# Kernel tuning notes

Hardware: AMD Instinct MI355X
Metric: run time of the kernel (lower is better)

## Reference

```python
import jax, jax.numpy as jnp
import numpy as np

B, S, D = 2, 2048, 1024
HEADS, HEAD_DIM = 16, 64

def setup_inputs() -> dict:
    key = jax.random.key(0)
    ks = jax.random.split(key, 5)
    sc = 0.02
    return {
        "hidden_states": jax.random.normal(ks[0], (B, S, D), jnp.float32),
        "Wq": jax.random.normal(ks[1], (D, HEADS * HEAD_DIM), jnp.float32) * sc,
        "Wk": jax.random.normal(ks[2], (D, HEADS * HEAD_DIM), jnp.float32) * sc,
        "Wv": jax.random.normal(ks[3], (D, HEADS * HEAD_DIM), jnp.float32) * sc,
        "Wo": jax.random.normal(ks[4], (HEADS * HEAD_DIM, D), jnp.float32) * sc,
        "bo": jnp.zeros((D,), jnp.float32),
    }

def reference(hidden_states, Wq, Wk, Wv, Wo, bo):
    b, s, _ = hidden_states.shape
    # QKV projections (no bias, as in diffusers Attention defaults)
    q = (hidden_states @ Wq).reshape(b, s, HEADS, HEAD_DIM).transpose(0, 2, 1, 3)
    k = (hidden_states @ Wk).reshape(b, s, HEADS, HEAD_DIM).transpose(0, 2, 1, 3)
    v = (hidden_states @ Wv).reshape(b, s, HEADS, HEAD_DIM).transpose(0, 2, 1, 3)
    scale = 1.0 / jnp.sqrt(jnp.asarray(HEAD_DIM, hidden_states.dtype))
    scores = jnp.einsum('bhqd,bhkd->bhqk', q, k) * scale  # full NxN scores
    attn = jax.nn.softmax(scores, axis=-1)
    out = jnp.einsum('bhqk,bhkd->bhqd', attn, v)
    out = out.transpose(0, 2, 1, 3).reshape(b, s, HEADS * HEAD_DIM)
    return out @ Wo + bo
```

## Files before the change

kernel.cpp:

```cpp
#include <hip/hip_runtime.h>

#define B_ 2
#define S_ 2048
#define D_ 1024
#define H_ 16
#define HD_ 64
#define M_ (B_ * S_)

typedef __attribute__((ext_vector_type(4))) float f32x4;
typedef __attribute__((ext_vector_type(16))) float f32x16;
typedef __attribute__((ext_vector_type(8))) short s16x8;
typedef unsigned short u16;
typedef unsigned int u32;

#define QSCALE 0.1803368801111204f

__device__ __forceinline__ u16 f2bf(float f) {
  unsigned u = __float_as_uint(f);
  u += 0x7fffu + ((u >> 16) & 1u);
  return (u16)(u >> 16);
}

__device__ __forceinline__ u32 cvtpk_bf16(float lo, float hi) {
  u32 r;
  asm("v_cvt_pk_bf16_f32 %0, %1, %2" : "=v"(r) : "v"(lo), "v"(hi));
  return r;
}

__device__ __forceinline__ void g2lds16(const u16* g, u16* l) {
  __builtin_amdgcn_global_load_lds((const __attribute__((address_space(1))) u32*)(g),
                                   (__attribute__((address_space(3))) u32*)(l), 16, 0, 0);
}

__global__ __launch_bounds__(256) void prep_kernel(
    const float* __restrict__ X, const float* __restrict__ Wq,
    const float* __restrict__ Wk, const float* __restrict__ Wv,
    const float* __restrict__ Wo, u16* __restrict__ Xb, u16* __restrict__ Wt0) {
  __shared__ float tile[32][33];
  const int id = blockIdx.x;
  if (id < 2048) {
    int i = (id * 256 + threadIdx.x) * 8;
    const float4 va = *(const float4*)(X + i);
    const float4 vb = *(const float4*)(X + i + 4);
    union { u32 u[4]; s16x8 v; } pk;
    pk.u[0] = cvtpk_bf16(va.x, va.y); pk.u[1] = cvtpk_bf16(va.z, va.w);
    pk.u[2] = cvtpk_bf16(vb.x, vb.y); pk.u[3] = cvtpk_bf16(vb.z, vb.w);
    *(s16x8*)(Xb + i) = pk.v;
    return;
  }
  const int id2 = id - 2048;
  const int z = id2 >> 10;
  const float* W = (z == 0) ? Wq : (z == 1) ? Wk : (z == 2) ? Wv : Wo;
  u16* Wt = Wt0 + (size_t)z * (D_ * D_);
  const float sc = (z == 0) ? QSCALE : 1.0f;
  const int tx = threadIdx.x & 31, ty = threadIdx.x >> 5;
  const int c0 = (id2 & 31) * 32, r0 = ((id2 >> 5) & 31) * 32;
#pragma unroll
  for (int j = 0; j < 32; j += 8)
    tile[ty + j][tx] = W[(size_t)(r0 + ty + j) * D_ + c0 + tx];
  __syncthreads();
#pragma unroll
  for (int j = 0; j < 32; j += 8)
    Wt[(size_t)(c0 + ty + j) * D_ + r0 + tx] = f2bf(tile[tx][ty + j] * sc);
}

__global__ __launch_bounds__(256) void gemm_qkv_kernel(
    const u16* __restrict__ Xb, const u16* __restrict__ WqT,
    const u16* __restrict__ WkT, const u16* __restrict__ WvT,
    u16* __restrict__ Qb, u16* __restrict__ Kb, u16* __restrict__ Vt) {
  __shared__ u16 As[2][128 * 32];
  __shared__ u16 Bs[2][128 * 32];
  const int tid = threadIdx.x;
  const int lane = tid & 63, wid = tid >> 6;
  const int wr = wid >> 1, wc = wid & 1;
  const int l15 = lane & 15, l4 = lane >> 4;
  const int bm = blockIdx.x * 128;
  const int bn128 = blockIdx.y;
  const int sel = bn128 >> 3;
  const u16* Wt = (sel == 0) ? WqT : (sel == 1) ? WkT : WvT;
  const int bn = (bn128 & 7) * 128;
  const int r0 = lane >> 2;
  const int c0 = lane & 3;

#define GSTAGE(buf, kt)                                                          \
  do {                                                                           \
    _Pragma("unroll") for (int j = 0; j < 2; ++j) {                              \
      const int row = (wid * 2 + j) * 16 + r0;                                   \
      g2lds16(Xb + (size_t)(bm + row) * D_ + (kt) + c0 * 8,                      \
              &As[buf][(wid * 2 + j) * 512]);                                    \
      g2lds16(Wt + (size_t)(bn + row) * D_ + (kt) + c0 * 8,                      \
              &Bs[buf][(wid * 2 + j) * 512]);                                    \
    }                                                                            \
  } while (0)

  f32x4 acc[4][4] = {};
  GSTAGE(0, 0);
  __syncthreads();
  int cur = 0;
  for (int kt = 0; kt < D_; kt += 32) {
    GSTAGE(cur ^ 1, (kt + 32) & (D_ - 1));
    s16x8 af[4], bfr[4];
#pragma unroll
    for (int i = 0; i < 4; ++i) af[i] = *(const s16x8*)&As[cur][(wr * 64 + i * 16 + l15) * 32 + l4 * 8];
#pragma unroll
    for (int j = 0; j < 4; ++j) bfr[j] = *(const s16x8*)&Bs[cur][(wc * 64 + j * 16 + l15) * 32 + l4 * 8];
#pragma unroll
    for (int i = 0; i < 4; ++i)
#pragma unroll
      for (int j = 0; j < 4; ++j)
        acc[i][j] = __builtin_amdgcn_mfma_f32_16x16x32_bf16(af[i], bfr[j], acc[i][j], 0, 0, 0);
    __syncthreads();
    cur ^= 1;
  }
#undef GSTAGE
#pragma unroll
  for (int i = 0; i < 4; ++i)
#pragma unroll
    for (int j = 0; j < 4; ++j)
#pragma unroll
      for (int r = 0; r < 4; ++r) {
        int m = bm + wr * 64 + i * 16 + l4 * 4 + r;
        int n = bn + wc * 64 + j * 16 + l15;
        int bb = m >> 11, s = m & (S_ - 1);
        int h = n >> 6, d = n & 63;
        u16 v = f2bf(acc[i][j][r]);
        size_t bhsel = (size_t)bb * H_ + h;
        if (sel == 0)      Qb[(bhsel * S_ + s) * HD_ + d] = v;
        else if (sel == 1) Kb[(bhsel * S_ + s) * HD_ + d] = v;
        else               Vt[(bhsel * HD_ + d) * S_ + s] = v;
      }
}

__global__ __launch_bounds__(512, 2) void attn_kernel(
    const u16* __restrict__ Qb, const u16* __restrict__ Kb,
    const u16* __restrict__ Vt, u16* __restrict__ Ob) {
  __shared__ char smem_raw[65536];
  typedef u16 (*lds_t)[2][4096];
  lds_t Ks = (lds_t)smem_raw;
  lds_t Vs = (lds_t)(smem_raw + 32768);
  const int tid = threadIdx.x;
  const int lane = tid & 63, wid = tid >> 6;
  const int qg = wid & 3, half = wid >> 2;
  const int l31 = lane & 31, hi = lane >> 5;
  const int id = blockIdx.x;
  const int bh = (id & 7) * 4 + (id >> 6);
  const int qx = (id >> 3) & 7;
  const size_t kbase = (size_t)bh * S_ * HD_;
  const size_t vbase = (size_t)bh * HD_ * S_;
  const int q0 = qx * 256 + qg * 64;
  const int r0 = lane >> 3;
  const int cs = ((lane & 7) ^ r0) * 8;
  const int kv0 = half << 10;

#define STAGE(buf, kvv)                                                          \
  do {                                                                           \
    _Pragma("unroll") for (int j = 0; j < 2; ++j) {                              \
      const int row = (qg * 2 + j) * 8 + r0;                                     \
      g2lds16(Kb + kbase + (size_t)((kvv) + row) * HD_ + cs,                     \
              &Ks[half][buf][(qg * 2 + j) * 512]);                               \
      g2lds16(Vt + vbase + (size_t)row * S_ + (kvv) + cs,                        \
              &Vs[half][buf][(qg * 2 + j) * 512]);                               \
    }                                                                            \
  } while (0)

  STAGE(0, kv0);

  s16x8 aqA[4], aqB[4];
#pragma unroll
  for (int kc = 0; kc < 4; ++kc) {
    aqA[kc] = *(const s16x8*)(Qb + kbase + (size_t)(q0 + l31) * HD_ + kc * 16 + hi * 8);
    aqB[kc] = *(const s16x8*)(Qb + kbase + (size_t)(q0 + 32 + l31) * HD_ + kc * 16 + hi * 8);
  }

  f32x16 accA0 = {}, accA1 = {}, accB0 = {}, accB1 = {};
  float lsA = 0.f, lsB = 0.f;

  int choff[4];
#pragma unroll
  for (int c = 0; c < 4; ++c) choff[c] = ((c * 2 + hi) ^ (l31 & 7)) * 8;

  __syncthreads();

  for (int t = 0; t < 16; ++t) {
    const int buf = t & 1;
    STAGE(buf ^ 1, kv0 + (((t + 1) & 15) << 6));

    f32x16 sA0 = {}, sA1 = {}, sB0 = {}, sB1 = {};
    __builtin_amdgcn_s_setprio(1);
#pragma unroll
    for (int kc = 0; kc < 4; ++kc) {
      const s16x8 ka0 = *(const s16x8*)&Ks[half][buf][(l31) * 64 + choff[kc]];
      const s16x8 ka1 = *(const s16x8*)&Ks[half][buf][(32 + l31) * 64 + choff[kc]];
      sA0 = __builtin_amdgcn_mfma_f32_32x32x16_bf16(ka0, aqA[kc], sA0, 0, 0, 0);
      sB0 = __builtin_amdgcn_mfma_f32_32x32x16_bf16(ka0, aqB[kc], sB0, 0, 0, 0);
      sA1 = __builtin_amdgcn_mfma_f32_32x32x16_bf16(ka1, aqA[kc], sA1, 0, 0, 0);
      sB1 = __builtin_amdgcn_mfma_f32_32x32x16_bf16(ka1, aqB[kc], sB1, 0, 0, 0);
    }
    __builtin_amdgcn_s_setprio(0);

    float tA = 0.f, tB = 0.f;
#pragma unroll
    for (int r = 0; r < 16; ++r) {
      sA0[r] = __builtin_amdgcn_exp2f(sA0[r]);
      sA1[r] = __builtin_amdgcn_exp2f(sA1[r]);
      sB0[r] = __builtin_amdgcn_exp2f(sB0[r]);
      sB1[r] = __builtin_amdgcn_exp2f(sB1[r]);
      tA += sA0[r] + sA1[r];
      tB += sB0[r] + sB1[r];
    }
    lsA += tA;
    lsB += tB;

    s16x8 paA[4], paB[4];
#pragma unroll
    for (int c = 0; c < 4; ++c) {
      const int rr = (c & 1) * 8;
      u32 a0, a1, b0, b1;
      if (c < 2) {
        a0 = cvtpk_bf16(sA0[rr + 0], sA0[rr + 1]);
        a1 = cvtpk_bf16(sA0[rr + 2], sA0[rr + 3]);
        b0 = cvtpk_bf16(sA0[rr + 4], sA0[rr + 5]);
        b1 = cvtpk_bf16(sA0[rr + 6], sA0[rr + 7]);
      } else {
        a0 = cvtpk_bf16(sA1[rr + 0], sA1[rr + 1]);
        a1 = cvtpk_bf16(sA1[rr + 2], sA1[rr + 3]);
        b0 = cvtpk_bf16(sA1[rr + 4], sA1[rr + 5]);
        b1 = cvtpk_bf16(sA1[rr + 6], sA1[rr + 7]);
      }
      asm volatile("v_permlane32_swap_b32 %0, %1" : "+v"(a0), "+v"(b0));
      asm volatile("v_permlane32_swap_b32 %0, %1" : "+v"(a1), "+v"(b1));
      union { u32 u[4]; s16x8 v; } pk;
      pk.u[0] = a0; pk.u[1] = a1; pk.u[2] = b0; pk.u[3] = b1;
      paA[c] = pk.v;
    }
#pragma unroll
    for (int c = 0; c < 4; ++c) {
      const int rr = (c & 1) * 8;
      u32 a0, a1, b0, b1;
      if (c < 2) {
        a0 = cvtpk_bf16(sB0[rr + 0], sB0[rr + 1]);
        a1 = cvtpk_bf16(sB0[rr + 2], sB0[rr + 3]);
        b0 = cvtpk_bf16(sB0[rr + 4], sB0[rr + 5]);
        b1 = cvtpk_bf16(sB0[rr + 6], sB0[rr + 7]);
      } else {
        a0 = cvtpk_bf16(sB1[rr + 0], sB1[rr + 1]);
        a1 = cvtpk_bf16(sB1[rr + 2], sB1[rr + 3]);
        b0 = cvtpk_bf16(sB1[rr + 4], sB1[rr + 5]);
        b1 = cvtpk_bf16(sB1[rr + 6], sB1[rr + 7]);
      }
      asm volatile("v_permlane32_swap_b32 %0, %1" : "+v"(a0), "+v"(b0));
      asm volatile("v_permlane32_swap_b32 %0, %1" : "+v"(a1), "+v"(b1));
      union { u32 u[4]; s16x8 v; } pk;
      pk.u[0] = a0; pk.u[1] = a1; pk.u[2] = b0; pk.u[3] = b1;
      paB[c] = pk.v;
    }

    __builtin_amdgcn_s_setprio(1);
#pragma unroll
    for (int c = 0; c < 4; ++c) {
      const s16x8 vb0 = *(const s16x8*)&Vs[half][buf][(l31) * 64 + choff[c]];
      const s16x8 vb1 = *(const s16x8*)&Vs[half][buf][(32 + l31) * 64 + choff[c]];
      accA0 = __builtin_amdgcn_mfma_f32_32x32x16_bf16(paA[c], vb0, accA0, 0, 0, 0);
      accB0 = __builtin_amdgcn_mfma_f32_32x32x16_bf16(paB[c], vb0, accB0, 0, 0, 0);
      accA1 = __builtin_amdgcn_mfma_f32_32x32x16_bf16(paA[c], vb1, accA1, 0, 0, 0);
      accB1 = __builtin_amdgcn_mfma_f32_32x32x16_bf16(paB[c], vb1, accB1, 0, 0, 0);
    }
    __builtin_amdgcn_s_setprio(0);

    __syncthreads();
  }
#undef STAGE

  lsA += __shfl_xor(lsA, 32);
  lsB += __shfl_xor(lsB, 32);
  const int bb = bh >> 4, h = bh & 15;
  float (*MB)[64][33] = (float(*)[64][33])smem_raw;

  if (half) {
#pragma unroll
    for (int r = 0; r < 16; ++r) {
      MB[qg][lane][r] = accA0[r];
      MB[qg][lane][16 + r] = accA1[r];
    }
    MB[qg][lane][32] = lsA;
  }
  __syncthreads();
  if (!half) {
    lsA += MB[qg][lane][32];
#pragma unroll
    for (int r = 0; r < 16; ++r) {
      accA0[r] += MB[qg][lane][r];
      accA1[r] += MB[qg][lane][16 + r];
    }
#pragma unroll
    for (int r = 0; r < 16; ++r) {
      const int qrow = (r & 3) + 8 * (r >> 2) + 4 * hi;
      const float rinv = 1.0f / __shfl(lsA, qrow);
      const int q = q0 + qrow;
      Ob[(size_t)(bb * S_ + q) * (H_ * HD_) + h * HD_ + l31] = f2bf(accA0[r] * rinv);
      Ob[(size_t)(bb * S_ + q) * (H_ * HD_) + h * HD_ + 32 + l31] = f2bf(accA1[r] * rinv);
    }
  }
  __syncthreads();
  if (half) {
#pragma unroll
    for (int r = 0; r < 16; ++r) {
      MB[qg][lane][r] = accB0[r];
      MB[qg][lane][16 + r] = accB1[r];
    }
    MB[qg][lane][32] = lsB;
  }
  __syncthreads();
  if (!half) {
    lsB += MB[qg][lane][32];
#pragma unroll
    for (int r = 0; r < 16; ++r) {
      accB0[r] += MB[qg][lane][r];
      accB1[r] += MB[qg][lane][16 + r];
    }
#pragma unroll
    for (int r = 0; r < 16; ++r) {
      const int qrow = (r & 3) + 8 * (r >> 2) + 4 * hi;
      const float rinv = 1.0f / __shfl(lsB, qrow);
      const int q = q0 + 32 + qrow;
      Ob[(size_t)(bb * S_ + q) * (H_ * HD_) + h * HD_ + l31] = f2bf(accB0[r] * rinv);
      Ob[(size_t)(bb * S_ + q) * (H_ * HD_) + h * HD_ + 32 + l31] = f2bf(accB1[r] * rinv);
    }
  }
}

__global__ __launch_bounds__(256, 2) void gemm_o_kernel(
    const u16* __restrict__ A, const u16* __restrict__ Bt,
    const float* __restrict__ bias, float* __restrict__ C) {
  __shared__ u16 As[2][128 * 32];
  __shared__ u16 Bs[2][64 * 32];
  const int tid = threadIdx.x;
  const int lane = tid & 63, wid = tid >> 6;
  const int l15 = lane & 15, l4 = lane >> 4;
  const int bm = blockIdx.x * 128;
  const int bn = blockIdx.y * 64;
  const int r0 = lane >> 2;
  const int c0 = lane & 3;

#define GSTAGE(buf, kt)                                                          \
  do {                                                                           \
    _Pragma("unroll") for (int j = 0; j < 2; ++j) {                              \
      const int row = (wid * 2 + j) * 16 + r0;                                   \
      g2lds16(A + (size_t)(bm + row) * D_ + (kt) + c0 * 8,                       \
              &As[buf][(wid * 2 + j) * 512]);                                    \
    }                                                                            \
    g2lds16(Bt + (size_t)(bn + wid * 16 + r0) * D_ + (kt) + c0 * 8,              \
            &Bs[buf][wid * 512]);                                                \
  } while (0)

  f32x4 acc[2][4] = {};
  GSTAGE(0, 0);
  __syncthreads();
  int cur = 0;
  for (int kt = 0; kt < D_; kt += 32) {
    GSTAGE(cur ^ 1, (kt + 32) & (D_ - 1));
    s16x8 af[2], bfr[4];
#pragma unroll
    for (int i = 0; i < 2; ++i) af[i] = *(const s16x8*)&As[cur][(wid * 32 + i * 16 + l15) * 32 + l4 * 8];
#pragma unroll
    for (int j = 0; j < 4; ++j) bfr[j] = *(const s16x8*)&Bs[cur][(j * 16 + l15) * 32 + l4 * 8];
#pragma unroll
    for (int i = 0; i < 2; ++i)
#pragma unroll
      for (int j = 0; j < 4; ++j)
        acc[i][j] = __builtin_amdgcn_mfma_f32_16x16x32_bf16(af[i], bfr[j], acc[i][j], 0, 0, 0);
    __syncthreads();
    cur ^= 1;
  }
#undef GSTAGE
#pragma unroll
  for (int i = 0; i < 2; ++i)
#pragma unroll
    for (int j = 0; j < 4; ++j)
#pragma unroll
      for (int r = 0; r < 4; ++r) {
        int m = bm + wid * 32 + i * 16 + l4 * 4 + r;
        int n = bn + j * 16 + l15;
        C[(size_t)m * D_ + n] = acc[i][j][r] + bias[n];
      }
}

extern "C" void kernel_launch(void* const* d_in, const int* in_sizes, int n_in,
                              void* d_out, int out_size, void* d_ws, size_t ws_size,
                              hipStream_t stream) {
  const float* X  = (const float*)d_in[0];
  const float* Wq = (const float*)d_in[1];
  const float* Wk = (const float*)d_in[2];
  const float* Wv = (const float*)d_in[3];
  const float* Wo = (const float*)d_in[4];
  const float* bo = (const float*)d_in[5];
  float* out = (float*)d_out;

  char* w = (char*)d_ws;
  u16* Xb  = (u16*)(w);
  u16* WT  = (u16*)(w + (8u << 20));
  u16* WqT = WT;
  u16* WkT = WT + (1u << 20);
  u16* WvT = WT + (2u << 20);
  u16* WoT = WT + (3u << 20);
  u16* Qb  = (u16*)(w + (16u << 20));
  u16* Kb  = (u16*)(w + (24u << 20));
  u16* Vt  = (u16*)(w + (32u << 20));
  u16* Ob  = (u16*)(w + (40u << 20));

  prep_kernel<<<6144, 256, 0, stream>>>(X, Wq, Wk, Wv, Wo, Xb, WT);
  gemm_qkv_kernel<<<dim3(32, 24), 256, 0, stream>>>(Xb, WqT, WkT, WvT, Qb, Kb, Vt);
  attn_kernel<<<256, 512, 0, stream>>>(Qb, Kb, Vt, Ob);
  gemm_o_kernel<<<dim3(32, 16), 256, 0, stream>>>(Ob, WoT, bo, out);
}
```

Measured before the change: 113.6 us.

## Compute softmax row sums via MFMA with ones and stage V transpose through LDS

The attention kernel drops the per-element VALU summation of exponentiated scores. Row sums are now accumulated by extra MFMA calls that multiply the bf16 probabilities by a vector of ones, and the final reduction reads the sums straight from the accumulator layout, so no shuffle is needed. The QKV GEMM epilogue for V now writes the transposed tile through swizzled shared memory and stores 16-byte coalesced rows instead of scattered 2-byte writes. The costs are two extra MFMAs per PV step, a larger LDS reduction buffer, and row sums taken from bf16-rounded probabilities rather than fp32 values.

```diff
diff --git a/kernel.cpp b/kernel.cpp
--- a/kernel.cpp
+++ b/kernel.cpp
@@ -68,8 +68,9 @@
     const u16* __restrict__ Xb, const u16* __restrict__ WqT,
     const u16* __restrict__ WkT, const u16* __restrict__ WvT,
     u16* __restrict__ Qb, u16* __restrict__ Kb, u16* __restrict__ Vt) {
-  __shared__ u16 As[2][128 * 32];
-  __shared__ u16 Bs[2][128 * 32];
+  __shared__ u16 ldsraw[16384];
+  u16 (*As)[4096] = (u16(*)[4096])ldsraw;
+  u16 (*Bs)[4096] = (u16(*)[4096])(ldsraw + 8192);
   const int tid = threadIdx.x;
   const int lane = tid & 63, wid = tid >> 6;
   const int wr = wid >> 1, wc = wid & 1;
@@ -113,22 +114,49 @@
     cur ^= 1;
   }
 #undef GSTAGE
-#pragma unroll
-  for (int i = 0; i < 4; ++i)
-#pragma unroll
-    for (int j = 0; j < 4; ++j)
-#pragma unroll
-      for (int r = 0; r < 4; ++r) {
-        int m = bm + wr * 64 + i * 16 + l4 * 4 + r;
-        int n = bn + wc * 64 + j * 16 + l15;
-        int bb = m >> 11, s = m & (S_ - 1);
-        int h = n >> 6, d = n & 63;
-        u16 v = f2bf(acc[i][j][r]);
-        size_t bhsel = (size_t)bb * H_ + h;
-        if (sel == 0)      Qb[(bhsel * S_ + s) * HD_ + d] = v;
-        else if (sel == 1) Kb[(bhsel * S_ + s) * HD_ + d] = v;
-        else               Vt[(bhsel * HD_ + d) * S_ + s] = v;
+
+  if (sel == 2) {
+    u16* T = ldsraw;
+#pragma unroll
+    for (int i = 0; i < 4; ++i)
+#pragma unroll
+      for (int j = 0; j < 4; ++j) {
+        const int n = wc * 64 + j * 16 + l15;
+        const int mcol = wr * 64 + i * 16 + l4 * 4;
+        ushort4 v;
+        v.x = f2bf(acc[i][j][0]); v.y = f2bf(acc[i][j][1]);
+        v.z = f2bf(acc[i][j][2]); v.w = f2bf(acc[i][j][3]);
+        const u32 off = (u32)((n * 128 + mcol) * 2) ^ (u32)((n & 7) << 4);
+        *(ushort4*)((char*)T + off) = v;
       }
+    __syncthreads();
+    const int bb = bm >> 11, sb = bm & (S_ - 1);
+    const int trow = tid >> 1;
+    const int h = (bn + trow) >> 6, d = (bn + trow) & 63;
+    u16* vdst = Vt + ((size_t)(bb * H_ + h) * HD_ + d) * S_ + sb;
+#pragma unroll
+    for (int k = 0; k < 8; ++k) {
+      const int mcol = (tid & 1) * 64 + k * 8;
+      const u32 off = (u32)((trow * 128 + mcol) * 2) ^ (u32)((trow & 7) << 4);
+      *(s16x8*)(vdst + mcol) = *(const s16x8*)((const char*)T + off);
+    }
+  } else {
+#pragma unroll
+    for (int i = 0; i < 4; ++i)
+#pragma unroll
+      for (int j = 0; j < 4; ++j)
+#pragma unroll
+        for (int r = 0; r < 4; ++r) {
+          int m = bm + wr * 64 + i * 16 + l4 * 4 + r;
+          int n = bn + wc * 64 + j * 16 + l15;
+          int bb = m >> 11, s = m & (S_ - 1);
+          int h = n >> 6, d = n & 63;
+          u16 v = f2bf(acc[i][j][r]);
+          size_t bhsel = (size_t)bb * H_ + h;
+          if (sel == 0) Qb[(bhsel * S_ + s) * HD_ + d] = v;
+          else          Kb[(bhsel * S_ + s) * HD_ + d] = v;
+        }
+  }
 }
 
 __global__ __launch_bounds__(512, 2) void attn_kernel(
@@ -172,8 +200,11 @@
     aqB[kc] = *(const s16x8*)(Qb + kbase + (size_t)(q0 + 32 + l31) * HD_ + kc * 16 + hi * 8);
   }
 
+  const short one_bf = (short)0x3F80;
+  const s16x8 ones8 = {one_bf, one_bf, one_bf, one_bf, one_bf, one_bf, one_bf, one_bf};
+
   f32x16 accA0 = {}, accA1 = {}, accB0 = {}, accB1 = {};
-  float lsA = 0.f, lsB = 0.f;
+  f32x16 lsaccA = {}, lsaccB = {};
 
   int choff[4];
 #pragma unroll
@@ -198,18 +229,13 @@
     }
     __builtin_amdgcn_s_setprio(0);
 
-    float tA = 0.f, tB = 0.f;
 #pragma unroll
     for (int r = 0; r < 16; ++r) {
       sA0[r] = __builtin_amdgcn_exp2f(sA0[r]);
       sA1[r] = __builtin_amdgcn_exp2f(sA1[r]);
       sB0[r] = __builtin_amdgcn_exp2f(sB0[r]);
       sB1[r] = __builtin_amdgcn_exp2f(sB1[r]);
-      tA += sA0[r] + sA1[r];
-      tB += sB0[r] + sB1[r];
-    }
-    lsA += tA;
-    lsB += tB;
+    }
 
     s16x8 paA[4], paB[4];
 #pragma unroll
@@ -264,6 +290,8 @@
       accB0 = __builtin_amdgcn_mfma_f32_32x32x16_bf16(paB[c], vb0, accB0, 0, 0, 0);
       accA1 = __builtin_amdgcn_mfma_f32_32x32x16_bf16(paA[c], vb1, accA1, 0, 0, 0);
       accB1 = __builtin_amdgcn_mfma_f32_32x32x16_bf16(paB[c], vb1, accB1, 0, 0, 0);
+      lsaccA = __builtin_amdgcn_mfma_f32_32x32x16_bf16(paA[c], ones8, lsaccA, 0, 0, 0);
+      lsaccB = __builtin_amdgcn_mfma_f32_32x32x16_bf16(paB[c], ones8, lsaccB, 0, 0, 0);
     }
     __builtin_amdgcn_s_setprio(0);
 
@@ -271,34 +299,28 @@
   }
 #undef STAGE
 
-  lsA += __shfl_xor(lsA, 32);
-  lsB += __shfl_xor(lsB, 32);
   const int bb = bh >> 4, h = bh & 15;
-  float (*MB)[64][33] = (float(*)[64][33])smem_raw;
+  float (*MB)[64][49] = (float(*)[64][49])smem_raw;
 
   if (half) {
 #pragma unroll
     for (int r = 0; r < 16; ++r) {
       MB[qg][lane][r] = accA0[r];
       MB[qg][lane][16 + r] = accA1[r];
-    }
-    MB[qg][lane][32] = lsA;
+      MB[qg][lane][32 + r] = lsaccA[r];
+    }
   }
   __syncthreads();
   if (!half) {
-    lsA += MB[qg][lane][32];
 #pragma unroll
     for (int r = 0; r < 16; ++r) {
-      accA0[r] += MB[qg][lane][r];
-      accA1[r] += MB[qg][lane][16 + r];
-    }
-#pragma unroll
-    for (int r = 0; r < 16; ++r) {
+      const float o0 = accA0[r] + MB[qg][lane][r];
+      const float o1 = accA1[r] + MB[qg][lane][16 + r];
+      const float rinv = 1.0f / (lsaccA[r] + MB[qg][lane][32 + r]);
       const int qrow = (r & 3) + 8 * (r >> 2) + 4 * hi;
-      const float rinv = 1.0f / __shfl(lsA, qrow);
       const int q = q0 + qrow;
-      Ob[(size_t)(bb * S_ + q) * (H_ * HD_) + h * HD_ + l31] = f2bf(accA0[r] * rinv);
-      Ob[(size_t)(bb * S_ + q) * (H_ * HD_) + h * HD_ + 32 + l31] = f2bf(accA1[r] * rinv);
+      Ob[(size_t)(bb * S_ + q) * (H_ * HD_) + h * HD_ + l31] = f2bf(o0 * rinv);
+      Ob[(size_t)(bb * S_ + q) * (H_ * HD_) + h * HD_ + 32 + l31] = f2bf(o1 * rinv);
     }
   }
   __syncthreads();
@@ -307,24 +329,20 @@
     for (int r = 0; r < 16; ++r) {
       MB[qg][lane][r] = accB0[r];
       MB[qg][lane][16 + r] = accB1[r];
-    }
-    MB[qg][lane][32] = lsB;
+      MB[qg][lane][32 + r] = lsaccB[r];
+    }
   }
   __syncthreads();
   if (!half) {
-    lsB += MB[qg][lane][32];
 #pragma unroll
     for (int r = 0; r < 16; ++r) {
-      accB0[r] += MB[qg][lane][r];
-      accB1[r] += MB[qg][lane][16 + r];
-    }
-#pragma unroll
-    for (int r = 0; r < 16; ++r) {
+      const float o0 = accB0[r] + MB[qg][lane][r];
+      const float o1 = accB1[r] + MB[qg][lane][16 + r];
+      const float rinv = 1.0f / (lsaccB[r] + MB[qg][lane][32 + r]);
       const int qrow = (r & 3) + 8 * (r >> 2) + 4 * hi;
-      const float rinv = 1.0f / __shfl(lsB, qrow);
       const int q = q0 + 32 + qrow;
-      Ob[(size_t)(bb * S_ + q) * (H_ * HD_) + h * HD_ + l31] = f2bf(accB0[r] * rinv);
-      Ob[(size_t)(bb * S_ + q) * (H_ * HD_) + h * HD_ + 32 + l31] = f2bf(accB1[r] * rinv);
+      Ob[(size_t)(bb * S_ + q) * (H_ * HD_) + h * HD_ + l31] = f2bf(o0 * rinv);
+      Ob[(size_t)(bb * S_ + q) * (H_ * HD_) + h * HD_ + 32 + l31] = f2bf(o1 * rinv);
     }
   }
 }
```

Result: faster. 110.5 us (-2.8%).
